# Kernel tuning notes

Measured on AMD Instinct MI355X. Metric: run time of the kernel, lower is better.

The kernel has to match this reference:

```python
import jax, jax.numpy as jnp
import numpy as np

N = 8192
IN_FEATS = 512
OUT_FEATS = 256
NEG_SLOPE = 0.01  # torch nn.LeakyReLU default


def setup_inputs() -> dict:
    key = jax.random.key(0)
    k_adj, k_feat, k_w, k_b, k_a1, k_a2 = jax.random.split(key, 6)
    adj_matrix = jax.random.uniform(k_adj, (N, N), dtype=jnp.float32)
    eye_matrix = jnp.eye(N, dtype=jnp.float32)  # identity adjacency, per AAGNN usage
    subgraph_feats = jax.random.normal(k_feat, (N, IN_FEATS), dtype=jnp.float32)
    node_mask = jnp.ones((N,), dtype=bool)
    # nn.Linear(in_feats, out_feats) params (kaiming-uniform-ish init scale)
    lim = 1.0 / np.sqrt(IN_FEATS)
    W = jax.random.uniform(k_w, (OUT_FEATS, IN_FEATS), minval=-lim, maxval=lim, dtype=jnp.float32)
    b = jax.random.uniform(k_b, (OUT_FEATS,), minval=-lim, maxval=lim, dtype=jnp.float32)
    # a_1, a_2 ~ torch.rand(1, out_feats)
    a_1 = jax.random.uniform(k_a1, (1, OUT_FEATS), dtype=jnp.float32)
    a_2 = jax.random.uniform(k_a2, (1, OUT_FEATS), dtype=jnp.float32)
    return {"adj_matrix": adj_matrix, "eye_matrix": eye_matrix,
            "subgraph_feats": subgraph_feats, "node_mask": node_mask,
            "W": W, "b": b, "a_1": a_1, "a_2": a_2}


def reference(adj_matrix, eye_matrix, subgraph_feats, node_mask, W, b, a_1, a_2):
    # z = Linear(subgraph_feats)  -> [N, out]
    z = subgraph_feats @ W.T + b
    zi = jnp.sum(a_1 * z, axis=1, keepdims=True)  # [N,1]
    zj = jnp.sum(a_2 * z, axis=1, keepdims=True)  # [N,1]
    # masked attention scores: adj*zi + adj*(eye*zj), leakyrelu, row softmax
    scores = jax.nn.leaky_relu(adj_matrix * zi + adj_matrix * (eye_matrix * zj),
                               negative_slope=NEG_SLOPE)
    att = jax.nn.softmax(scores, axis=1)  # [N,N]
    h = z - att @ z  # [N, out]
    out = jax.nn.relu(h)
    # original returns relu(h[node_mask]); mask is all-True -> same rows, static shape
    return jnp.where(node_mask[:, None], out, 0.0)
```

## Files before the change

kernel.cpp:

```cpp
#include <hip/hip_runtime.h>

#define N_NODES 8192
#define IN_F 512
#define OUT_F 256
#define KSPLIT 8
#define KCHUNK (N_NODES / KSPLIT)

typedef float f32x4 __attribute__((ext_vector_type(4)));
typedef short short8 __attribute__((ext_vector_type(8)));
typedef short short4v __attribute__((ext_vector_type(4)));

__device__ __forceinline__ unsigned short f2bf(float f) {
  unsigned int u = __float_as_uint(f);
  return (unsigned short)((u + 0x8000u) >> 16);
}

__device__ __forceinline__ float bf2f(unsigned short b) {
  return __uint_as_float(((unsigned int)b) << 16);
}

__device__ __forceinline__ short8 pack8(const float4& a, const float4& b) {
  short8 r;
  r[0] = (short)f2bf(a.x); r[1] = (short)f2bf(a.y);
  r[2] = (short)f2bf(a.z); r[3] = (short)f2bf(a.w);
  r[4] = (short)f2bf(b.x); r[5] = (short)f2bf(b.y);
  r[6] = (short)f2bf(b.z); r[7] = (short)f2bf(b.w);
  return r;
}

__global__ __launch_bounds__(256) void zgemm_mfma(
    const float* __restrict__ feats, const float* __restrict__ W,
    const float* __restrict__ bias, const float* __restrict__ a1v,
    const float* __restrict__ a2v, float* __restrict__ z,
    unsigned short* __restrict__ zF, float* __restrict__ zi_out,
    float* __restrict__ zj_out) {
  __shared__ float zred[4][32][2];
  const int tid = threadIdx.x;
  const int w = tid >> 6;
  const int l = tid & 63;
  const int g4 = l >> 4;
  const int gm = l & 15;
  const int ib = blockIdx.x * 32;

  f32x4 acc[2][4];
#pragma unroll
  for (int a = 0; a < 2; ++a)
#pragma unroll
    for (int b = 0; b < 4; ++b) acc[a][b] = (f32x4){0.f, 0.f, 0.f, 0.f};

#pragma unroll 2
  for (int ks = 0; ks < 16; ++ks) {
    const int k0 = ks * 32 + g4 * 8;
    short8 afr[2], bfr[4];
#pragma unroll
    for (int it = 0; it < 2; ++it) {
      const float* p = &feats[(size_t)(ib + it * 16 + gm) * IN_F + k0];
      afr[it] = pack8(*(const float4*)p, *(const float4*)(p + 4));
    }
#pragma unroll
    for (int nt = 0; nt < 4; ++nt) {
      const float* p = &W[(size_t)(w * 64 + nt * 16 + gm) * IN_F + k0];
      bfr[nt] = pack8(*(const float4*)p, *(const float4*)(p + 4));
    }
#pragma unroll
    for (int it = 0; it < 2; ++it)
#pragma unroll
      for (int nt = 0; nt < 4; ++nt)
        acc[it][nt] = __builtin_amdgcn_mfma_f32_16x16x32_bf16(
            afr[it], bfr[nt], acc[it][nt], 0, 0, 0);
  }

  const int kb = ib >> 5;
  float pzi[8] = {}, pzj[8] = {};
#pragma unroll
  for (int ntz = 0; ntz < 4; ++ntz) {
    const int col = w * 64 + ntz * 16 + gm;
    const float bv = bias[col];
    const float A1 = a1v[col], A2 = a2v[col];
    const int nt = w * 4 + ntz;
#pragma unroll
    for (int it = 0; it < 2; ++it) {
      short4v q;
#pragma unroll
      for (int r = 0; r < 4; ++r) {
        const int row = ib + it * 16 + g4 * 4 + r;
        const float v = acc[it][ntz][r] + bv;
        z[(size_t)row * OUT_F + col] = v;
        q[r] = (short)f2bf(v);
        pzi[it * 4 + r] += A1 * v;
        pzj[it * 4 + r] += A2 * v;
      }
      const int lane = (it * 2 + (g4 >> 1)) * 16 + gm;
      const int eb = (g4 & 1) * 4;
      *(short4v*)&zF[(size_t)(nt * 256 + kb) * 512 + lane * 8 + eb] = q;
    }
  }
#pragma unroll
  for (int off = 1; off < 16; off <<= 1)
#pragma unroll
    for (int q = 0; q < 8; ++q) {
      pzi[q] += __shfl_xor(pzi[q], off);
      pzj[q] += __shfl_xor(pzj[q], off);
    }
  if (gm == 0) {
#pragma unroll
    for (int it = 0; it < 2; ++it)
#pragma unroll
      for (int r = 0; r < 4; ++r) {
        zred[w][it * 16 + g4 * 4 + r][0] = pzi[it * 4 + r];
        zred[w][it * 16 + g4 * 4 + r][1] = pzj[it * 4 + r];
      }
  }
  __syncthreads();
  if (tid < 64) {
    const int row = tid >> 1, which = tid & 1;
    const float s = zred[0][row][which] + zred[1][row][which] +
                    zred[2][row][which] + zred[3][row][which];
    if (which == 0) zi_out[ib + row] = s;
    else zj_out[ib + row] = s;
  }
}

__global__ __launch_bounds__(256) void p_kernel(
    const float* __restrict__ adj, const float* __restrict__ zi_in,
    const float* __restrict__ zj_in, unsigned short* __restrict__ Pn,
    float* __restrict__ l_ws) {
  __shared__ float red[4];
  const int row = blockIdx.x;
  const int tid = threadIdx.x;
  const float zir = zi_in[row];
  const float zjr = zj_in[row];
  const float* rp = adj + (size_t)row * N_NODES + tid * 4;

  f32x4 a[8];
#pragma unroll
  for (int c = 0; c < 8; ++c)
    a[c] = __builtin_nontemporal_load((const f32x4*)(rp + c * 1024));

  float psum = 0.f;
  unsigned short* op = Pn + (size_t)row * N_NODES + tid * 4;
#pragma unroll
  for (int c = 0; c < 8; ++c) {
    short4v v;
#pragma unroll
    for (int e = 0; e < 4; ++e) {
      const int j = c * 1024 + tid * 4 + e;
      const float av = a[c][e];
      float s = av * zir;
      if (j == row) s += av * zjr;
      s = fmaxf(s, 0.01f * s);
      const unsigned short pb = f2bf(__expf(s));
      psum += bf2f(pb);
      v[e] = (short)pb;
    }
    *(short4v*)(op + c * 1024) = v;
  }

#pragma unroll
  for (int off = 32; off > 0; off >>= 1) psum += __shfl_xor(psum, off);
  if ((tid & 63) == 0) red[tid >> 6] = psum;
  __syncthreads();
  if (tid == 0) l_ws[row] = red[0] + red[1] + red[2] + red[3];
}

__global__ __launch_bounds__(256, 3) void pz_gemm(
    const unsigned short* __restrict__ Pn,
    const unsigned short* __restrict__ zF, float* __restrict__ acc_ws) {
  __shared__ __align__(16) unsigned short Pt[2][64][64];
  const int tid = threadIdx.x;
  const int w = tid >> 6;
  const int l = tid & 63;
  const int l4 = l >> 4;
  const int lm = l & 15;
  const int mt = blockIdx.x & 127;
  const int kc = blockIdx.x >> 7;
  const int ib = mt * 64;
  const int jb0 = kc * KCHUNK;

  f32x4 acc[4][4];
#pragma unroll
  for (int a = 0; a < 4; ++a)
#pragma unroll
    for (int b = 0; b < 4; ++b) acc[a][b] = (f32x4){0.f, 0.f, 0.f, 0.f};

  const int NST = KCHUNK / 64;

#pragma unroll
  for (int m = 0; m < 2; ++m) {
    const int g = m * 256 + tid, r = g >> 3, s = g & 7;
    *(short8*)&Pt[0][r][(s ^ (r & 7)) * 8] =
        *(const short8*)&Pn[(size_t)(ib + r) * N_NODES + jb0 + s * 8];
  }

  for (int st = 0; st < NST; ++st) {
    const int b = st & 1;
    __syncthreads();

    short8 pg[2];
    if (st + 1 < NST) {
      const int jb = jb0 + (st + 1) * 64;
#pragma unroll
      for (int m = 0; m < 2; ++m) {
        const int g = m * 256 + tid, r = g >> 3, s = g & 7;
        pg[m] = *(const short8*)&Pn[(size_t)(ib + r) * N_NODES + jb + s * 8];
      }
    }

    const int kb0 = (jb0 + st * 64) >> 5;
    short8 bfr[2][4];
#pragma unroll
    for (int kk = 0; kk < 2; ++kk)
#pragma unroll
      for (int ntz = 0; ntz < 4; ++ntz)
        bfr[kk][ntz] = *(const short8*)&zF[(size_t)((w * 4 + ntz) * 256 +
                                                    kb0 + kk) * 512 + l * 8];

#pragma unroll
    for (int it = 0; it < 4; ++it) {
      const int r = it * 16 + lm;
#pragma unroll
      for (int kk = 0; kk < 2; ++kk) {
        const short8 afr =
            *(const short8*)&Pt[b][r][((kk * 4 + l4) ^ (r & 7)) * 8];
#pragma unroll
        for (int ntz = 0; ntz < 4; ++ntz)
          acc[it][ntz] = __builtin_amdgcn_mfma_f32_16x16x32_bf16(
              afr, bfr[kk][ntz], acc[it][ntz], 0, 0, 0);
      }
    }

    __syncthreads();

    if (st + 1 < NST) {
#pragma unroll
      for (int m = 0; m < 2; ++m) {
        const int g = m * 256 + tid, r = g >> 3, s = g & 7;
        *(short8*)&Pt[b ^ 1][r][(s ^ (r & 7)) * 8] = pg[m];
      }
    }
  }

#pragma unroll
  for (int it = 0; it < 4; ++it)
#pragma unroll
    for (int nt = 0; nt < 4; ++nt)
#pragma unroll
      for (int r = 0; r < 4; ++r) {
        const int gi = ib + it * 16 + l4 * 4 + r;
        const int gn = w * 64 + nt * 16 + lm;
        acc_ws[((size_t)kc * N_NODES + gi) * OUT_F + gn] = acc[it][nt][r];
      }
}

__global__ void finalize_kernel(const float* __restrict__ z,
                                const float* __restrict__ acc_ws,
                                const float* __restrict__ l_ws,
                                float* __restrict__ out) {
  const int i = blockIdx.x;
  const int n = threadIdx.x;
  const float ls = l_ws[i];
  float a = 0.f;
#pragma unroll
  for (int kc = 0; kc < KSPLIT; ++kc)
    a += acc_ws[((size_t)kc * N_NODES + i) * OUT_F + n];
  const float v = z[(size_t)i * OUT_F + n] - a / ls;
  out[(size_t)i * OUT_F + n] = fmaxf(v, 0.f);
}

extern "C" void kernel_launch(void* const* d_in, const int* in_sizes, int n_in,
                              void* d_out, int out_size, void* d_ws,
                              size_t ws_size, hipStream_t stream) {
  (void)in_sizes; (void)n_in; (void)out_size; (void)ws_size;
  const float* adj = (const float*)d_in[0];
  const float* feats = (const float*)d_in[2];
  const float* W = (const float*)d_in[4];
  const float* bias = (const float*)d_in[5];
  const float* a1v = (const float*)d_in[6];
  const float* a2v = (const float*)d_in[7];
  float* out = (float*)d_out;

  char* ws = (char*)d_ws;
  float* z = (float*)ws;
  unsigned short* zF = (unsigned short*)(ws + ((size_t)8 << 20));
  float* zi = (float*)(ws + ((size_t)12 << 20));
  float* zj = zi + N_NODES;
  float* l_ws = (float*)(ws + ((size_t)13 << 20));
  float* acc_ws = (float*)(ws + ((size_t)16 << 20));
  unsigned short* Pn = (unsigned short*)(ws + ((size_t)96 << 20));

  hipLaunchKernelGGL(zgemm_mfma, dim3(N_NODES / 32), dim3(256), 0, stream,
                     feats, W, bias, a1v, a2v, z, zF, zi, zj);
  hipLaunchKernelGGL(p_kernel, dim3(N_NODES), dim3(256), 0, stream, adj, zi,
                     zj, Pn, l_ws);
  hipLaunchKernelGGL(pz_gemm, dim3(128 * KSPLIT), dim3(256), 0, stream, Pn,
                     zF, acc_ws);
  hipLaunchKernelGGL(finalize_kernel, dim3(N_NODES), dim3(256), 0, stream, z,
                     acc_ws, l_ws, out);
}
```

Before: 149.4 us.

## Stage P tiles via direct global-to-LDS loads and vectorize finalize

The P tile staging in the P·z GEMM switches from register-staged global loads plus LDS stores to direct global_load_lds DMA into the swizzled shared buffer. The next stage is issued before compute, which removes one barrier and the register round trip. Occupancy hint goes from 3 to 4 blocks per CU. The finalize kernel now processes four columns per thread with 128-bit loads and stores. Risk: the async LDS writes rely on the single trailing barrier for ordering, and the swizzle mapping must match the reader's pattern.

```diff
diff --git a/kernel.cpp b/kernel.cpp
--- a/kernel.cpp
+++ b/kernel.cpp
@@ -26,6 +26,13 @@
   r[4] = (short)f2bf(b.x); r[5] = (short)f2bf(b.y);
   r[6] = (short)f2bf(b.z); r[7] = (short)f2bf(b.w);
   return r;
+}
+
+__device__ __forceinline__ void gload_lds16(const unsigned short* g,
+                                            unsigned short* l) {
+  __builtin_amdgcn_global_load_lds(
+      (const __attribute__((address_space(1))) unsigned int*)g,
+      (__attribute__((address_space(3))) unsigned int*)l, 16, 0, 0);
 }
 
 __global__ __launch_bounds__(256) void zgemm_mfma(
@@ -163,7 +170,7 @@
   if (tid == 0) l_ws[row] = red[0] + red[1] + red[2] + red[3];
 }
 
-__global__ __launch_bounds__(256, 3) void pz_gemm(
+__global__ __launch_bounds__(256, 4) void pz_gemm(
     const unsigned short* __restrict__ Pn,
     const unsigned short* __restrict__ zF, float* __restrict__ acc_ws) {
   __shared__ __align__(16) unsigned short Pt[2][64][64];
@@ -177,6 +184,9 @@
   const int ib = mt * 64;
   const int jb0 = kc * KCHUNK;
 
+  const int srow = l >> 3;
+  const int schk = (l & 7) ^ srow;
+
   f32x4 acc[4][4];
 #pragma unroll
   for (int a = 0; a < 4; ++a)
@@ -185,26 +195,22 @@
 
   const int NST = KCHUNK / 64;
 
-#pragma unroll
-  for (int m = 0; m < 2; ++m) {
-    const int g = m * 256 + tid, r = g >> 3, s = g & 7;
-    *(short8*)&Pt[0][r][(s ^ (r & 7)) * 8] =
-        *(const short8*)&Pn[(size_t)(ib + r) * N_NODES + jb0 + s * 8];
-  }
+#define STAGE(buf, jb)                                                      \
+  {                                                                         \
+    _Pragma("unroll") for (int m = 0; m < 2; ++m) {                         \
+      const int g = w * 2 + m;                                              \
+      gload_lds16(                                                          \
+          &Pn[(size_t)(ib + g * 8 + srow) * N_NODES + (jb) + schk * 8],     \
+          &Pt[buf][0][0] + g * 512);                                        \
+    }                                                                       \
+  }
+
+  STAGE(0, jb0);
+  __syncthreads();
 
   for (int st = 0; st < NST; ++st) {
     const int b = st & 1;
-    __syncthreads();
-
-    short8 pg[2];
-    if (st + 1 < NST) {
-      const int jb = jb0 + (st + 1) * 64;
-#pragma unroll
-      for (int m = 0; m < 2; ++m) {
-        const int g = m * 256 + tid, r = g >> 3, s = g & 7;
-        pg[m] = *(const short8*)&Pn[(size_t)(ib + r) * N_NODES + jb + s * 8];
-      }
-    }
+    if (st + 1 < NST) STAGE(b ^ 1, jb0 + (st + 1) * 64);
 
     const int kb0 = (jb0 + st * 64) >> 5;
     short8 bfr[2][4];
@@ -230,14 +236,6 @@
     }
 
     __syncthreads();
-
-    if (st + 1 < NST) {
-#pragma unroll
-      for (int m = 0; m < 2; ++m) {
-        const int g = m * 256 + tid, r = g >> 3, s = g & 7;
-        *(short8*)&Pt[b ^ 1][r][(s ^ (r & 7)) * 8] = pg[m];
-      }
-    }
   }
 
 #pragma unroll
@@ -256,15 +254,19 @@
                                 const float* __restrict__ acc_ws,
                                 const float* __restrict__ l_ws,
                                 float* __restrict__ out) {
-  const int i = blockIdx.x;
-  const int n = threadIdx.x;
+  const int t = blockIdx.x * 256 + threadIdx.x;
+  const int i = t >> 6;
+  const int c = (t & 63) * 4;
   const float ls = l_ws[i];
-  float a = 0.f;
+  f32x4 a = (f32x4){0.f, 0.f, 0.f, 0.f};
 #pragma unroll
   for (int kc = 0; kc < KSPLIT; ++kc)
-    a += acc_ws[((size_t)kc * N_NODES + i) * OUT_F + n];
-  const float v = z[(size_t)i * OUT_F + n] - a / ls;
-  out[(size_t)i * OUT_F + n] = fmaxf(v, 0.f);
+    a += *(const f32x4*)&acc_ws[((size_t)kc * N_NODES + i) * OUT_F + c];
+  const f32x4 zv = *(const f32x4*)&z[(size_t)i * OUT_F + c];
+  f32x4 r;
+#pragma unroll
+  for (int e = 0; e < 4; ++e) r[e] = fmaxf(zv[e] - a[e] / ls, 0.f);
+  *(f32x4*)&out[(size_t)i * OUT_F + c] = r;
 }
 
 extern "C" void kernel_launch(void* const* d_in, const int* in_sizes, int n_in,
@@ -294,6 +296,6 @@
                      zj, Pn, l_ws);
   hipLaunchKernelGGL(pz_gemm, dim3(128 * KSPLIT), dim3(256), 0, stream, Pn,
                      zF, acc_ws);
-  hipLaunchKernelGGL(finalize_kernel, dim3(N_NODES), dim3(256), 0, stream, z,
-                     acc_ws, l_ws, out);
-}
+  hipLaunchKernelGGL(finalize_kernel, dim3(N_NODES * OUT_F / 1024), dim3(256),
+                     0, stream, z, acc_ws, l_ws, out);
+}
```

After: 152.5 us. 2.1% more time.
